# Kernel tuning notes

Hardware: AMD Instinct MI355X
Metric: run time of the kernel (lower is better)

## Reference

```python
import jax, jax.numpy as jnp
import numpy as np

V, E, H, T, B, F, D = 50000, 300, 256, 512, 64, 128, 256


def setup_inputs() -> dict:
    key = jax.random.key(0)
    ks = jax.random.split(key, 28)
    def g(i, shape, s=0.05):
        return jax.random.normal(ks[i], shape, jnp.float32) * s
    return {
        "tokens": jax.random.randint(ks[0], (B, T), 0, V, dtype=jnp.int32),
        "lengths": jax.random.randint(ks[1], (B,), 16, T + 1, dtype=jnp.int32),
        "emb": g(2, (V, E), 0.1),
        "Wih_f": g(3, (4 * H, E)), "Whh_f": g(4, (4 * H, H)),
        "bih_f": g(5, (4 * H,)), "bhh_f": g(6, (4 * H,)),
        "Wih_b": g(7, (4 * H, E)), "Whh_b": g(8, (4 * H, H)),
        "bih_b": g(9, (4 * H,)), "bhh_b": g(10, (4 * H,)),
        "attn_w": g(11, (2 * H, 1)), "attn_b": g(12, (1,)),
        "conv_w3": g(13, (F, 2 * H, 3)), "conv_b3": g(14, (F,)),
        "conv_w5": g(15, (F, 2 * H, 5)), "conv_b5": g(16, (F,)),
        "conv_w7": g(17, (F, 2 * H, 7)), "conv_b7": g(18, (F,)),
        "conv_w9": g(19, (F, 2 * H, 9)), "conv_b9": g(20, (F,)),
        "fc1_w": g(21, (D, 4 * F)), "fc1_b": g(22, (D,)),
        "fc2_w": g(23, (1, D)), "fc2_b": g(24, (1,)),
    }


def _lstm(x, Wih, Whh, bih, bhh):
    # x: [T, B, E]; torch LSTM gate order i, f, g, o. Returns hidden states [T, B, H].
    Hd = Whh.shape[1]
    xg = jnp.einsum('tbe,ge->tbg', x, Wih) + bih + bhh  # precompute input projections
    def step(carry, g_t):
        h, c = carry
        g = g_t + h @ Whh.T
        i, f, gg, o = jnp.split(g, 4, axis=-1)
        c = jax.nn.sigmoid(f) * c + jax.nn.sigmoid(i) * jnp.tanh(gg)
        h = jax.nn.sigmoid(o) * jnp.tanh(c)
        return (h, c), h
    h0 = jnp.zeros((x.shape[1], Hd), x.dtype)
    _, hs = jax.lax.scan(step, (h0, h0), xg)
    return hs


def _conv1d(x, w, b):
    # x: [B, C, T], w: [F, C, k] -> [B, F, T-k+1]
    y = jax.lax.conv_general_dilated(x, w, (1,), 'VALID',
                                     dimension_numbers=('NCH', 'OIH', 'NCH'))
    return y + b[None, :, None]


def reference(tokens, lengths, emb, Wih_f, Whh_f, bih_f, bhh_f,
              Wih_b, Whh_b, bih_b, bhh_b, attn_w, attn_b,
              conv_w3, conv_b3, conv_w5, conv_b5, conv_w7, conv_b7,
              conv_w9, conv_b9, fc1_w, fc1_b, fc2_w, fc2_b):
    Tn = tokens.shape[1]
    x = emb[tokens].transpose(1, 0, 2)                         # [T, B, E]
    t_idx = jnp.arange(Tn)
    mask = (t_idx[:, None] < lengths[None, :]).astype(x.dtype)  # [T, B]
    # forward direction
    fwd = _lstm(x, Wih_f, Whh_f, bih_f, bhh_f)
    # backward direction: per-sequence reverse of the valid prefix (packed-sequence semantics)
    rev = jnp.where(mask > 0, lengths[None, :] - 1 - t_idx[:, None], t_idx[:, None])  # [T, B]
    x_rev = jnp.take_along_axis(x, rev[:, :, None], axis=0)
    bwd = jnp.take_along_axis(_lstm(x_rev, Wih_b, Whh_b, bih_b, bhh_b), rev[:, :, None], axis=0)
    h = jnp.concatenate([fwd, bwd], axis=-1)                   # [T, B, 2H]
    # per-sequence softmax attention over valid timesteps (exp-normalize as in source)
    u = jnp.tanh(h) @ attn_w + attn_b                          # [T, B, 1]
    e = jnp.exp(u[..., 0]) * mask                              # [T, B]
    ctx = e / jnp.sum(e, axis=0, keepdims=True)
    r = h * ctx[..., None]                                     # zero at padded steps -> ZeroPad2d to max_len
    cnn_in = r.transpose(1, 2, 0)                              # [B, 2H, max_len]
    pooled = [jnp.max(_conv1d(cnn_in, w, b), axis=-1)
              for w, b in ((conv_w3, conv_b3), (conv_w5, conv_b5),
                           (conv_w7, conv_b7), (conv_w9, conv_b9))]
    cat = jnp.concatenate(pooled, axis=1)                      # [B, 4F]
    out = jax.nn.relu(cat @ fc1_w.T + fc1_b)
    out = jax.nn.sigmoid(out @ fc2_w.T + fc2_b)
    return out.reshape(-1, 1)
```

## Files before the change

kernel.cpp:

```cpp
#include <hip/hip_runtime.h>
#include <stdint.h>

typedef __attribute__((ext_vector_type(4))) float f32x4;
typedef __attribute__((ext_vector_type(8))) short s16x8;
typedef __attribute__((ext_vector_type(4))) unsigned short us4;

__device__ __forceinline__ float b2f(unsigned short h) {
    union { unsigned int u; float f; } v; v.u = ((unsigned int)h) << 16; return v.f;
}
__device__ __forceinline__ unsigned short f2b(float f) {
    union { float f; unsigned int u; } v; v.f = f;
    unsigned int u = v.u;
    unsigned int r = (u + 0x7FFFu + ((u >> 16) & 1u)) >> 16;
    return (unsigned short)r;
}
__device__ __forceinline__ f32x4 mfma_bf16(s16x8 a, s16x8 b, f32x4 c) {
    return __builtin_amdgcn_mfma_f32_16x16x32_bf16(a, b, c, 0, 0, 0);
}
__device__ __forceinline__ float fast_rcp(float x) {
    return __builtin_amdgcn_rcpf(x);
}
__device__ __forceinline__ float sigm(float x) {
    return fast_rcp(1.f + __expf(-x));
}
__device__ __forceinline__ float tanh_ap(float x) {
    float e = __expf(2.f * x);
    return 1.f - 2.f * fast_rcp(e + 1.f);
}
__device__ __forceinline__ unsigned int mapf(float f) {
    union { float f; unsigned int u; } v; v.f = f;
    return (v.u & 0x80000000u) ? ~v.u : (v.u | 0x80000000u);
}

#define TT 512
#define BB 64
#define EE 300
#define EPAD 320
#define HH 256
#define G4 1024
#define TP 520

__global__ void prep_w(const float* __restrict__ Wih_f, const float* __restrict__ Wih_b,
                       const float* __restrict__ Whh_f, const float* __restrict__ Whh_b,
                       const float* __restrict__ bih_f, const float* __restrict__ bhh_f,
                       const float* __restrict__ bih_b, const float* __restrict__ bhh_b,
                       unsigned short* __restrict__ Wb_f, unsigned short* __restrict__ Wb_b,
                       unsigned short* __restrict__ Whhb_f, unsigned short* __restrict__ Whhb_b,
                       float* __restrict__ bias_f, float* __restrict__ bias_b)
{
    int idx = blockIdx.x * 256 + threadIdx.x;
    if (idx < 327680) {
        int n = idx / EPAD, k = idx % EPAD;
        Wb_f[idx] = f2b(k < EE ? Wih_f[n * EE + k] : 0.f);
    } else if (idx < 655360) {
        int i = idx - 327680; int n = i / EPAD, k = i % EPAD;
        Wb_b[i] = f2b(k < EE ? Wih_b[n * EE + k] : 0.f);
    } else if (idx < 917504) {
        int i = idx - 655360; Whhb_f[i] = f2b(Whh_f[i]);
    } else if (idx < 1179648) {
        int i = idx - 917504; Whhb_b[i] = f2b(Whh_b[i]);
    } else if (idx < 1180672) {
        int i = idx - 1179648; bias_f[i] = bih_f[i] + bhh_f[i];
    } else if (idx < 1181696) {
        int i = idx - 1180672; bias_b[i] = bih_b[i] + bhh_b[i];
    }
}

__global__ void wcat_prep(const float* __restrict__ w3, const float* __restrict__ w5,
                          const float* __restrict__ w7, const float* __restrict__ w9,
                          unsigned short* __restrict__ Wcat)
{
    int idx = blockIdx.x * 256 + threadIdx.x;
    if (idx >= 512 * 4608) return;
    int f = idx / 4608, kk = idx - f * 4608;
    int j = kk >> 9, c = kk & 511;
    int g = f >> 7, fl = f & 127;
    int kw = 3 + 2 * g;
    const float* src = (g == 0) ? w3 : ((g == 1) ? w5 : ((g == 2) ? w7 : w9));
    float v = (j < kw) ? src[((size_t)fl * 512 + c) * kw + j] : 0.f;
    Wcat[idx] = f2b(v);
}

__global__ void build_A(const int* __restrict__ tokens, const int* __restrict__ lengths,
                        const float* __restrict__ emb,
                        unsigned short* __restrict__ A_f, unsigned short* __restrict__ A_b)
{
    int idx = blockIdx.x * 256 + threadIdx.x;
    const int per = 32768 * 40;
    if (idx >= 2 * per) return;
    int dirc = idx >= per;
    int rem = dirc ? idx - per : idx;
    int row = rem / 40, kc = (rem - row * 40) * 8;
    int t = row >> 6, b = row & 63;
    int ts = t;
    if (dirc) { int len = lengths[b]; ts = (t < len) ? (len - 1 - t) : t; }
    int tok = tokens[b * TT + ts];
    const float* ep = emb + (size_t)tok * EE;
    unsigned short* dst = (dirc ? A_b : A_f) + (size_t)row * EPAD + kc;
#pragma unroll
    for (int j2 = 0; j2 < 8; ++j2) {
        int e = kc + j2;
        dst[j2] = f2b(e < EE ? ep[e] : 0.f);
    }
}

__global__ void pool_init(unsigned int* __restrict__ p) {
    int idx = blockIdx.x * 256 + threadIdx.x;
    if (idx < 64 * 512) p[idx] = 0x007FFFFFu;
}

__global__ void zero_r(unsigned short* __restrict__ r) {
    int idx = blockIdx.x * 256 + threadIdx.x;
    if (idx >= 64 * 8 * 512) return;
    int b = idx >> 12;
    int rem = idx & 4095;
    r[((size_t)b * TP + 512) * 512 + rem] = 0;
}

__global__ __launch_bounds__(256) void gemm_xg_k(
    const unsigned short* __restrict__ A, const unsigned short* __restrict__ Bw,
    const float* __restrict__ bias, unsigned short* __restrict__ C)
{
    __shared__ unsigned short As[128][72];
    __shared__ unsigned short Bs[128][72];
    const int KA = EPAD;
    int tid = threadIdx.x;
    int row0 = blockIdx.x * 128, col0 = blockIdx.y * 128;
    int lane = tid & 63, wave = tid >> 6;
    int wr = (wave >> 1) * 64, wc = (wave & 1) * 64;
    int l15 = lane & 15, lg = lane >> 4;
    f32x4 acc[4][4] = {};
    for (int k0 = 0; k0 < KA; k0 += 64) {
        for (int ci = tid; ci < 1024; ci += 256) {
            int rr = ci >> 3, kc = (ci & 7) * 8;
            *(s16x8*)(&As[rr][kc]) = *(const s16x8*)(A + (size_t)(row0 + rr) * KA + k0 + kc);
            *(s16x8*)(&Bs[rr][kc]) = *(const s16x8*)(Bw + (size_t)(col0 + rr) * KA + k0 + kc);
        }
        __syncthreads();
#pragma unroll
        for (int kk = 0; kk < 64; kk += 32) {
            s16x8 af[4], bf[4];
#pragma unroll
            for (int m = 0; m < 4; ++m) af[m] = *(const s16x8*)(&As[wr + m * 16 + l15][kk + lg * 8]);
#pragma unroll
            for (int n = 0; n < 4; ++n) bf[n] = *(const s16x8*)(&Bs[wc + n * 16 + l15][kk + lg * 8]);
#pragma unroll
            for (int m = 0; m < 4; ++m)
#pragma unroll
                for (int n = 0; n < 4; ++n)
                    acc[m][n] = mfma_bf16(af[m], bf[n], acc[m][n]);
        }
        __syncthreads();
    }
    int t = (row0 + wr) >> 6;
#pragma unroll
    for (int m = 0; m < 4; ++m)
#pragma unroll
        for (int n = 0; n < 4; ++n) {
            int ccol = col0 + wc + n * 16 + l15;
            float bb = bias[ccol];
            us4 pk;
#pragma unroll
            for (int i = 0; i < 4; ++i) pk[i] = f2b(acc[m][n][i] + bb);
            size_t us4_idx = (((size_t)t * 4 + m) * 1024 + ccol) * 4 + lg;
            *(us4*)(C + us4_idx * 4) = pk;
        }
}

#define LSTM_STEP(S, XCUR, XNXT, HC, HW)                                          \
{                                                                                 \
    _Pragma("unroll")                                                             \
    for (int ct = 0; ct < 8; ++ct)                                                \
        wl2a[ct] = *(const s16x8*)(wbase + coff[ct] + 6 * 32);                    \
    f32x4 acc[8];                                                                 \
    _Pragma("unroll")                                                             \
    for (int ct = 0; ct < 8; ++ct) {                                              \
        f32x4 a;                                                                  \
        _Pragma("unroll")                                                         \
        for (int i = 0; i < 4; ++i) a[i] = b2f(XCUR[ct][i]);                      \
        acc[ct] = a;                                                              \
    }                                                                             \
    __syncthreads();              \
    s16x8 af[8];                                                                  \
    _Pragma("unroll")                                                             \
    for (int kt = 0; kt < 8; ++kt) af[kt] = *(const s16x8*)((HC) + kt * 32);      \
    _Pragma("unroll")                                                             \
    for (int kt = 0; kt < 4; ++kt)                                                \
        _Pragma("unroll")                                                         \
        for (int ct = 0; ct < 8; ++ct)                                            \
            acc[ct] = mfma_bf16(af[kt], wreg[ct * 4 + kt], acc[ct]);              \
    _Pragma("unroll")                                                             \
    for (int ct = 0; ct < 8; ++ct)                                                \
        wl2b[ct] = *(const s16x8*)(wbase + coff[ct] + 7 * 32);                    \
    _Pragma("unroll")                                                             \
    for (int ktl = 0; ktl < 2; ++ktl)                                             \
        _Pragma("unroll")                                                         \
        for (int ct = 0; ct < 8; ++ct)                                            \
            acc[ct] = mfma_bf16(af[4 + ktl], w_lds[wave][ktl][ct][lane], acc[ct]);\
    {                                                                             \
        int sp1 = (S) + 1; if (sp1 > 511) sp1 = 511;                              \
        const unsigned short* xs = xbase + (size_t)sp1 * 65536;                   \
        XNXT[0] = *(const us4*)(xs);                                              \
        XNXT[1] = *(const us4*)(xs + 256);                                        \
        XNXT[2] = *(const us4*)(xs + 4096);                                       \
        XNXT[3] = *(const us4*)(xs + 4352);                                       \
        XNXT[4] = *(const us4*)(xs + 8192);                                       \
        XNXT[5] = *(const us4*)(xs + 8448);                                       \
        XNXT[6] = *(const us4*)(xs + 12288);                                      \
        XNXT[7] = *(const us4*)(xs + 12544);                                      \
    }                                                                             \
    _Pragma("unroll")                                                             \
    for (int ct = 0; ct < 8; ++ct) acc[ct] = mfma_bf16(af[6], wl2a[ct], acc[ct]); \
    _Pragma("unroll")                                                             \
    for (int ct = 0; ct < 8; ++ct) acc[ct] = mfma_bf16(af[7], wl2b[ct], acc[ct]); \
    _Pragma("unroll")                                                             \
    for (int h2 = 0; h2 < 2; ++h2)                                                \
    _Pragma("unroll")                                                             \
    for (int i = 0; i < 4; ++i) {                                                 \
        int bi = lg * 4 + i;                                                      \
        int u = wave * 32 + h2 * 16 + l15;                                        \
        float gi = acc[0 + h2][i], gf = acc[2 + h2][i];                           \
        float gg = acc[4 + h2][i], go = acc[6 + h2][i];                           \
        float si = sigm(gi), sf = sigm(gf), so = sigm(go);                        \
        float tg = tanh_ap(gg);                                                   \
        int q = h2 * 4 + i;                                                       \
        float cc = sf * c[q] + si * tg; c[q] = cc;                                \
        float hh = so * tanh_ap(cc);                                              \
        (HW)[bi][u] = f2b(hh);                                                    \
        int len = len_s[bi];                                                      \
        if ((S) < len) {                                                          \
            int t_out = dir ? (len - 1 - (S)) : (S);                              \
            hs[((size_t)t_out * 64 + (grp * 16 + bi)) * 512 + dir * 256 + u] = f2b(hh); \
        }                                                                         \
    }                                                                             \
}

__global__ __launch_bounds__(512, 2) void lstm_rec(
    const unsigned short* __restrict__ xg_f, const unsigned short* __restrict__ xg_b,
    const unsigned short* __restrict__ Whh_fb, const unsigned short* __restrict__ Whh_bb,
    const int* __restrict__ lengths, unsigned short* __restrict__ hs)
{
    int wg = blockIdx.x;
    int dir = wg >> 2, grp = wg & 3;
    const unsigned short* XG = dir ? xg_b : xg_f;
    const unsigned short* WH = dir ? Whh_bb : Whh_fb;
    int tid = threadIdx.x, lane = tid & 63, wave = tid >> 6;
    int l15 = lane & 15, lg = lane >> 4;

    __shared__ unsigned short h_a[2][16][264];
    __shared__ s16x8 w_lds[8][2][8][64];
    __shared__ int len_s[16];
    __shared__ int ml_s;

    if (tid < 16) len_s[tid] = lengths[grp * 16 + tid];
    for (int i = tid; i < 2 * 16 * 264; i += 512) (&h_a[0][0][0])[i] = 0;
    __syncthreads();
    if (tid == 0) {
        int m = 0;
        for (int i = 0; i < 16; ++i) m = max(m, len_s[i]);
        ml_s = m;
    }

    const unsigned short* wbase = WH + (size_t)(wave * 32 + l15) * HH + lg * 8;
    const int coff[8] = {0, 16 * HH, 256 * HH, 272 * HH, 512 * HH, 528 * HH, 768 * HH, 784 * HH};

    s16x8 wreg[32];
#pragma unroll
    for (int ct = 0; ct < 8; ++ct) {
#pragma unroll
        for (int kt = 0; kt < 4; ++kt)
            wreg[ct * 4 + kt] = *(const s16x8*)(wbase + coff[ct] + kt * 32);
#pragma unroll
        for (int ktl = 0; ktl < 2; ++ktl)
            w_lds[wave][ktl][ct][lane] = *(const s16x8*)(wbase + coff[ct] + (4 + ktl) * 32);
    }
    __syncthreads();
    int maxlen = ml_s;

    float c[8];
#pragma unroll
    for (int q = 0; q < 8; ++q) c[q] = 0.f;

    const unsigned short* hc0 = &h_a[0][l15][lg * 8];
    const unsigned short* hc1 = &h_a[1][l15][lg * 8];
    const unsigned short* xbase = XG + (size_t)grp * 16384 + (wave * 32 + l15) * 16 + lg * 4;

    s16x8 wl2a[8], wl2b[8];
    us4 xga[8], xgb[8];
    {
        const unsigned short* xs = xbase;
        xga[0] = *(const us4*)(xs);         xga[1] = *(const us4*)(xs + 256);
        xga[2] = *(const us4*)(xs + 4096);  xga[3] = *(const us4*)(xs + 4352);
        xga[4] = *(const us4*)(xs + 8192);  xga[5] = *(const us4*)(xs + 8448);
        xga[6] = *(const us4*)(xs + 12288); xga[7] = *(const us4*)(xs + 12544);
    }

    int s = 0;
    for (; s + 1 < maxlen; s += 2) {
        LSTM_STEP(s, xga, xgb, hc0, h_a[1])
        LSTM_STEP(s + 1, xgb, xga, hc1, h_a[0])
    }
    if (s < maxlen) {
        LSTM_STEP(s, xga, xgb, hc0, h_a[1])
    }
}

__global__ __launch_bounds__(256) void attn_k(
    const unsigned short* __restrict__ hs, const int* __restrict__ lengths,
    const float* __restrict__ attn_w, unsigned short* __restrict__ r)
{
    int b = blockIdx.x, tid = threadIdx.x;
    __shared__ float aw[512];
    __shared__ float e_s[512];
    __shared__ float red[4];
    __shared__ float ssum;
    for (int i = tid; i < 512; i += 256) aw[i] = attn_w[i];
    int len = lengths[b];
    __syncthreads();
    for (int t = tid; t < 512; t += 256) {
        float e = 0.f;
        if (t < len) {
            const unsigned short* hp = hs + ((size_t)t * 64 + b) * 512;
            float u = 0.f;
            for (int c8 = 0; c8 < 64; ++c8) {
                s16x8 hv = *(const s16x8*)(hp + c8 * 8);
#pragma unroll
                for (int j = 0; j < 8; ++j)
                    u += tanh_ap(b2f((unsigned short)hv[j])) * aw[c8 * 8 + j];
            }
            e = __expf(u);
        }
        e_s[t] = e;
    }
    __syncthreads();
    float p = e_s[tid] + e_s[tid + 256];
#pragma unroll
    for (int o = 32; o > 0; o >>= 1) p += __shfl_down(p, o);
    if ((tid & 63) == 0) red[tid >> 6] = p;
    __syncthreads();
    if (tid == 0) ssum = red[0] + red[1] + red[2] + red[3];
    __syncthreads();
    float inv = fast_rcp(ssum);
    for (int idx = tid; idx < 512 * 512; idx += 256) {
        int t = idx >> 9, c = idx & 511;
        unsigned short outv = 0;
        if (t < len) {
            float scale = e_s[t] * inv;
            outv = f2b(b2f(hs[((size_t)t * 64 + b) * 512 + c]) * scale);
        }
        r[((size_t)b * TP + t) * 512 + c] = outv;
    }
}

__global__ __launch_bounds__(256) void gemm_conv(
    const unsigned short* __restrict__ R, const unsigned short* __restrict__ W,
    unsigned int* __restrict__ pooled)
{
    __shared__ unsigned short As[128][72];
    __shared__ unsigned short Bs[128][72];
    int tid = threadIdx.x;
    int bm = blockIdx.x;
    int b = bm >> 2;
    int t0 = (bm & 3) * 128;
    int col0 = blockIdx.y * 128;
    int kmax = (3 + 2 * (int)blockIdx.y) * 512;
    int lane = tid & 63, wave = tid >> 6;
    int wr = (wave >> 1) * 64, wc = (wave & 1) * 64;
    int l15 = lane & 15, lg = lane >> 4;
    f32x4 acc[4][4] = {};
    for (int k0 = 0; k0 < kmax; k0 += 64) {
        int j = k0 >> 9, c0 = k0 & 511;
        for (int ci = tid; ci < 1024; ci += 256) {
            int rr = ci >> 3, kc = (ci & 7) * 8;
            *(s16x8*)(&As[rr][kc]) =
                *(const s16x8*)(R + ((size_t)(b * TP) + t0 + rr + j) * 512 + c0 + kc);
            *(s16x8*)(&Bs[rr][kc]) = *(const s16x8*)(W + (size_t)(col0 + rr) * 4608 + k0 + kc);
        }
        __syncthreads();
#pragma unroll
        for (int kk = 0; kk < 64; kk += 32) {
            s16x8 af[4], bf[4];
#pragma unroll
            for (int m = 0; m < 4; ++m) af[m] = *(const s16x8*)(&As[wr + m * 16 + l15][kk + lg * 8]);
#pragma unroll
            for (int n = 0; n < 4; ++n) bf[n] = *(const s16x8*)(&Bs[wc + n * 16 + l15][kk + lg * 8]);
#pragma unroll
            for (int m = 0; m < 4; ++m)
#pragma unroll
                for (int n = 0; n < 4; ++n)
                    acc[m][n] = mfma_bf16(af[m], bf[n], acc[m][n]);
        }
        __syncthreads();
    }
#pragma unroll
    for (int m = 0; m < 4; ++m)
#pragma unroll
        for (int n = 0; n < 4; ++n) {
            int f = col0 + wc + n * 16 + l15;
            int g = f >> 7;
            int tmax = 509 - 2 * g;
            float v = -3.4e38f;
            int tb = t0 + wr + m * 16 + lg * 4;
#pragma unroll
            for (int i = 0; i < 4; ++i) {
                int t = tb + i;
                if (t <= tmax) v = fmaxf(v, acc[m][n][i]);
            }
            v = fmaxf(v, __shfl_xor(v, 16));
            v = fmaxf(v, __shfl_xor(v, 32));
            if (lane < 16) atomicMax(&pooled[b * 512 + f], mapf(v));
        }
}

__global__ __launch_bounds__(256) void fc_k(
    const unsigned int* __restrict__ pooled,
    const float* __restrict__ cb3, const float* __restrict__ cb5,
    const float* __restrict__ cb7, const float* __restrict__ cb9,
    const float* __restrict__ fc1_w, const float* __restrict__ fc1_b,
    const float* __restrict__ fc2_w, const float* __restrict__ fc2_b,
    float* __restrict__ out)
{
    int b = blockIdx.x, tid = threadIdx.x;
    __shared__ float x[512];
    __shared__ float y[256];
    for (int i = tid; i < 512; i += 256) {
        unsigned int u = pooled[b * 512 + i];
        unsigned int bits = (u & 0x80000000u) ? (u & 0x7FFFFFFFu) : ~u;
        union { unsigned int uu; float f; } v; v.uu = bits;
        int g = i >> 7;
        const float* cb = (g == 0) ? cb3 : ((g == 1) ? cb5 : ((g == 2) ? cb7 : cb9));
        x[i] = v.f + cb[i & 127];
    }
    __syncthreads();
    float a = fc1_b[tid];
    const float* wrow = fc1_w + (size_t)tid * 512;
    for (int k = 0; k < 512; k += 4)
        a += x[k] * wrow[k] + x[k + 1] * wrow[k + 1] + x[k + 2] * wrow[k + 2] + x[k + 3] * wrow[k + 3];
    y[tid] = fmaxf(a, 0.f);
    __syncthreads();
    if (tid < 64) {
        float p = 0.f;
        for (int k = tid; k < 256; k += 64) p += y[k] * fc2_w[k];
#pragma unroll
        for (int o = 32; o > 0; o >>= 1) p += __shfl_down(p, o);
        if (tid == 0) out[b] = 1.f / (1.f + __expf(-(p + fc2_b[0])));
    }
}

extern "C" void kernel_launch(void* const* d_in, const int* in_sizes, int n_in,
                              void* d_out, int out_size, void* d_ws, size_t ws_size,
                              hipStream_t stream)
{
    const int*   tokens  = (const int*)d_in[0];
    const int*   lengths = (const int*)d_in[1];
    const float* emb     = (const float*)d_in[2];
    const float* Wih_f   = (const float*)d_in[3];
    const float* Whh_f   = (const float*)d_in[4];
    const float* bih_f   = (const float*)d_in[5];
    const float* bhh_f   = (const float*)d_in[6];
    const float* Wih_b   = (const float*)d_in[7];
    const float* Whh_b   = (const float*)d_in[8];
    const float* bih_b   = (const float*)d_in[9];
    const float* bhh_b   = (const float*)d_in[10];
    const float* attn_w  = (const float*)d_in[11];
    const float* cw3 = (const float*)d_in[13]; const float* cb3 = (const float*)d_in[14];
    const float* cw5 = (const float*)d_in[15]; const float* cb5 = (const float*)d_in[16];
    const float* cw7 = (const float*)d_in[17]; const float* cb7 = (const float*)d_in[18];
    const float* cw9 = (const float*)d_in[19]; const float* cb9 = (const float*)d_in[20];
    const float* fc1_w = (const float*)d_in[21]; const float* fc1_b = (const float*)d_in[22];
    const float* fc2_w = (const float*)d_in[23]; const float* fc2_b = (const float*)d_in[24];
    float* out = (float*)d_out;

    char* ws = (char*)d_ws;
    unsigned short* A_f    = (unsigned short*)(ws + 0);
    unsigned short* A_b    = (unsigned short*)(ws + 20971520);
    unsigned short* r      = (unsigned short*)(ws + 0);
    unsigned short* Wb_f   = (unsigned short*)(ws + 41943040);
    unsigned short* Wb_b   = (unsigned short*)(ws + 42598400);
    unsigned short* Whhb_f = (unsigned short*)(ws + 43253760);
    unsigned short* Whhb_b = (unsigned short*)(ws + 43778048);
    float*          bias_f = (float*)(ws + 44302336);
    float*          bias_b = (float*)(ws + 44306432);
    unsigned short* Wcat   = (unsigned short*)(ws + 44310528);
    unsigned int*   pooled = (unsigned int*)(ws + 49029120);
    unsigned short* xg_f   = (unsigned short*)(ws + 49160192);
    unsigned short* xg_b   = (unsigned short*)(ws + 116269056);
    unsigned short* hs     = (unsigned short*)(ws + 183377920);

    prep_w<<<(1181696 + 255) / 256, 256, 0, stream>>>(Wih_f, Wih_b, Whh_f, Whh_b,
        bih_f, bhh_f, bih_b, bhh_b, Wb_f, Wb_b, Whhb_f, Whhb_b, bias_f, bias_b);
    wcat_prep<<<(2359296 + 255) / 256, 256, 0, stream>>>(cw3, cw5, cw7, cw9, Wcat);
    build_A<<<(2621440 + 255) / 256, 256, 0, stream>>>(tokens, lengths, emb, A_f, A_b);
    pool_init<<<128, 256, 0, stream>>>(pooled);

    gemm_xg_k<<<dim3(256, 8), 256, 0, stream>>>(A_f, Wb_f, bias_f, xg_f);
    gemm_xg_k<<<dim3(256, 8), 256, 0, stream>>>(A_b, Wb_b, bias_b, xg_b);

    lstm_rec<<<8, 512, 0, stream>>>(xg_f, xg_b, Whhb_f, Whhb_b, lengths, hs);

    zero_r<<<(262144 + 255) / 256, 256, 0, stream>>>(r);
    attn_k<<<64, 256, 0, stream>>>(hs, lengths, attn_w, r);

    gemm_conv<<<dim3(256, 4), 256, 0, stream>>>(r, Wcat, pooled);

    fc_k<<<64, 256, 0, stream>>>(pooled, cb3, cb5, cb7, cb9,
                                 fc1_w, fc1_b, fc2_w, fc2_b, out);
}
```

Baseline: 2.180 ms.

## Split LSTM recurrence across 16 waves with 16 hidden units each

Doubles the lstm_rec workgroup from 512 to 1024 threads so each wave owns 16 hidden units (4 gate tiles) instead of 32 (8 gate tiles). Each wave then issues half as many MFMAs and loads per timestep, which shortens the serial per-step critical path of the recurrence. The cost is more waves contending at the per-step barrier. Register budget per thread must also fit the higher launch bound, which could force spills.

```diff
diff --git a/kernel.cpp b/kernel.cpp
--- a/kernel.cpp
+++ b/kernel.cpp
@@ -170,11 +170,11 @@
 #define LSTM_STEP(S, XCUR, XNXT, HC, HW)                                          \
 {                                                                                 \
     _Pragma("unroll")                                                             \
-    for (int ct = 0; ct < 8; ++ct)                                                \
-        wl2a[ct] = *(const s16x8*)(wbase + coff[ct] + 6 * 32);                    \
-    f32x4 acc[8];                                                                 \
-    _Pragma("unroll")                                                             \
-    for (int ct = 0; ct < 8; ++ct) {                                              \
+    for (int ct = 0; ct < 4; ++ct)                                                \
+        wl2a[ct] = *(const s16x8*)(wbase + ct * 65536 + 6 * 32);                  \
+    f32x4 acc[4];                                                                 \
+    _Pragma("unroll")                                                             \
+    for (int ct = 0; ct < 4; ++ct) {                                              \
         f32x4 a;                                                                  \
         _Pragma("unroll")                                                         \
         for (int i = 0; i < 4; ++i) a[i] = b2f(XCUR[ct][i]);                      \
@@ -187,55 +187,46 @@
     _Pragma("unroll")                                                             \
     for (int kt = 0; kt < 4; ++kt)                                                \
         _Pragma("unroll")                                                         \
-        for (int ct = 0; ct < 8; ++ct)                                            \
+        for (int ct = 0; ct < 4; ++ct)                                            \
             acc[ct] = mfma_bf16(af[kt], wreg[ct * 4 + kt], acc[ct]);              \
     _Pragma("unroll")                                                             \
-    for (int ct = 0; ct < 8; ++ct)                                                \
-        wl2b[ct] = *(const s16x8*)(wbase + coff[ct] + 7 * 32);                    \
+    for (int ct = 0; ct < 4; ++ct)                                                \
+        wl2b[ct] = *(const s16x8*)(wbase + ct * 65536 + 7 * 32);                  \
     _Pragma("unroll")                                                             \
     for (int ktl = 0; ktl < 2; ++ktl)                                             \
         _Pragma("unroll")                                                         \
-        for (int ct = 0; ct < 8; ++ct)                                            \
+        for (int ct = 0; ct < 4; ++ct)                                            \
             acc[ct] = mfma_bf16(af[4 + ktl], w_lds[wave][ktl][ct][lane], acc[ct]);\
     {                                                                             \
         int sp1 = (S) + 1; if (sp1 > 511) sp1 = 511;                              \
         const unsigned short* xs = xbase + (size_t)sp1 * 65536;                   \
         XNXT[0] = *(const us4*)(xs);                                              \
-        XNXT[1] = *(const us4*)(xs + 256);                                        \
-        XNXT[2] = *(const us4*)(xs + 4096);                                       \
-        XNXT[3] = *(const us4*)(xs + 4352);                                       \
-        XNXT[4] = *(const us4*)(xs + 8192);                                       \
-        XNXT[5] = *(const us4*)(xs + 8448);                                       \
-        XNXT[6] = *(const us4*)(xs + 12288);                                      \
-        XNXT[7] = *(const us4*)(xs + 12544);                                      \
+        XNXT[1] = *(const us4*)(xs + 4096);                                       \
+        XNXT[2] = *(const us4*)(xs + 8192);                                       \
+        XNXT[3] = *(const us4*)(xs + 12288);                                      \
     }                                                                             \
     _Pragma("unroll")                                                             \
-    for (int ct = 0; ct < 8; ++ct) acc[ct] = mfma_bf16(af[6], wl2a[ct], acc[ct]); \
-    _Pragma("unroll")                                                             \
-    for (int ct = 0; ct < 8; ++ct) acc[ct] = mfma_bf16(af[7], wl2b[ct], acc[ct]); \
-    _Pragma("unroll")                                                             \
-    for (int h2 = 0; h2 < 2; ++h2)                                                \
+    for (int ct = 0; ct < 4; ++ct) acc[ct] = mfma_bf16(af[6], wl2a[ct], acc[ct]); \
+    _Pragma("unroll")                                                             \
+    for (int ct = 0; ct < 4; ++ct) acc[ct] = mfma_bf16(af[7], wl2b[ct], acc[ct]); \
     _Pragma("unroll")                                                             \
     for (int i = 0; i < 4; ++i) {                                                 \
         int bi = lg * 4 + i;                                                      \
-        int u = wave * 32 + h2 * 16 + l15;                                        \
-        float gi = acc[0 + h2][i], gf = acc[2 + h2][i];                           \
-        float gg = acc[4 + h2][i], go = acc[6 + h2][i];                           \
+        float gi = acc[0][i], gf = acc[1][i], gg = acc[2][i], go = acc[3][i];     \
         float si = sigm(gi), sf = sigm(gf), so = sigm(go);                        \
         float tg = tanh_ap(gg);                                                   \
-        int q = h2 * 4 + i;                                                       \
-        float cc = sf * c[q] + si * tg; c[q] = cc;                                \
+        float cc = sf * c[i] + si * tg; c[i] = cc;                                \
         float hh = so * tanh_ap(cc);                                              \
-        (HW)[bi][u] = f2b(hh);                                                    \
+        (HW)[bi][u_col] = f2b(hh);                                                \
         int len = len_s[bi];                                                      \
         if ((S) < len) {                                                          \
             int t_out = dir ? (len - 1 - (S)) : (S);                              \
-            hs[((size_t)t_out * 64 + (grp * 16 + bi)) * 512 + dir * 256 + u] = f2b(hh); \
+            hs[((size_t)t_out * 64 + (grp * 16 + bi)) * 512 + dir * 256 + u_col] = f2b(hh); \
         }                                                                         \
     }                                                                             \
 }
 
-__global__ __launch_bounds__(512, 2) void lstm_rec(
+__global__ __launch_bounds__(1024, 4) void lstm_rec(
     const unsigned short* __restrict__ xg_f, const unsigned short* __restrict__ xg_b,
     const unsigned short* __restrict__ Whh_fb, const unsigned short* __restrict__ Whh_bb,
     const int* __restrict__ lengths, unsigned short* __restrict__ hs)
@@ -246,14 +237,15 @@
     const unsigned short* WH = dir ? Whh_bb : Whh_fb;
     int tid = threadIdx.x, lane = tid & 63, wave = tid >> 6;
     int l15 = lane & 15, lg = lane >> 4;
+    int u_col = wave * 16 + l15;
 
     __shared__ unsigned short h_a[2][16][264];
-    __shared__ s16x8 w_lds[8][2][8][64];
+    __shared__ s16x8 w_lds[16][2][4][64];
     __shared__ int len_s[16];
     __shared__ int ml_s;
 
     if (tid < 16) len_s[tid] = lengths[grp * 16 + tid];
-    for (int i = tid; i < 2 * 16 * 264; i += 512) (&h_a[0][0][0])[i] = 0;
+    for (int i = tid; i < 2 * 16 * 264; i += 1024) (&h_a[0][0][0])[i] = 0;
     __syncthreads();
     if (tid == 0) {
         int m = 0;
@@ -261,38 +253,37 @@
         ml_s = m;
     }
 
-    const unsigned short* wbase = WH + (size_t)(wave * 32 + l15) * HH + lg * 8;
-    const int coff[8] = {0, 16 * HH, 256 * HH, 272 * HH, 512 * HH, 528 * HH, 768 * HH, 784 * HH};
-
-    s16x8 wreg[32];
-#pragma unroll
-    for (int ct = 0; ct < 8; ++ct) {
+    const unsigned short* wbase = WH + (size_t)u_col * HH + lg * 8;
+
+    s16x8 wreg[16];
+#pragma unroll
+    for (int ct = 0; ct < 4; ++ct) {
 #pragma unroll
         for (int kt = 0; kt < 4; ++kt)
-            wreg[ct * 4 + kt] = *(const s16x8*)(wbase + coff[ct] + kt * 32);
+            wreg[ct * 4 + kt] = *(const s16x8*)(wbase + ct * 65536 + kt * 32);
 #pragma unroll
         for (int ktl = 0; ktl < 2; ++ktl)
-            w_lds[wave][ktl][ct][lane] = *(const s16x8*)(wbase + coff[ct] + (4 + ktl) * 32);
+            w_lds[wave][ktl][ct][lane] = *(const s16x8*)(wbase + ct * 65536 + (4 + ktl) * 32);
     }
     __syncthreads();
     int maxlen = ml_s;
 
-    float c[8];
-#pragma unroll
-    for (int q = 0; q < 8; ++q) c[q] = 0.f;
+    float c[4];
+#pragma unroll
+    for (int q = 0; q < 4; ++q) c[q] = 0.f;
 
     const unsigned short* hc0 = &h_a[0][l15][lg * 8];
     const unsigned short* hc1 = &h_a[1][l15][lg * 8];
-    const unsigned short* xbase = XG + (size_t)grp * 16384 + (wave * 32 + l15) * 16 + lg * 4;
-
-    s16x8 wl2a[8], wl2b[8];
-    us4 xga[8], xgb[8];
+    const unsigned short* xbase = XG + (size_t)grp * 16384 + (size_t)u_col * 16 + lg * 4;
+
+    s16x8 wl2a[4], wl2b[4];
+    us4 xga[4], xgb[4];
     {
         const unsigned short* xs = xbase;
-        xga[0] = *(const us4*)(xs);         xga[1] = *(const us4*)(xs + 256);
-        xga[2] = *(const us4*)(xs + 4096);  xga[3] = *(const us4*)(xs + 4352);
-        xga[4] = *(const us4*)(xs + 8192);  xga[5] = *(const us4*)(xs + 8448);
-        xga[6] = *(const us4*)(xs + 12288); xga[7] = *(const us4*)(xs + 12544);
+        xga[0] = *(const us4*)(xs);
+        xga[1] = *(const us4*)(xs + 4096);
+        xga[2] = *(const us4*)(xs + 8192);
+        xga[3] = *(const us4*)(xs + 12288);
     }
 
     int s = 0;
@@ -496,7 +487,7 @@
     gemm_xg_k<<<dim3(256, 8), 256, 0, stream>>>(A_f, Wb_f, bias_f, xg_f);
     gemm_xg_k<<<dim3(256, 8), 256, 0, stream>>>(A_b, Wb_b, bias_b, xg_b);
 
-    lstm_rec<<<8, 512, 0, stream>>>(xg_f, xg_b, Whhb_f, Whhb_b, lengths, hs);
+    lstm_rec<<<8, 1024, 0, stream>>>(xg_f, xg_b, Whhb_f, Whhb_b, lengths, hs);
 
     zero_r<<<(262144 + 255) / 256, 256, 0, stream>>>(r);
     attn_k<<<64, 256, 0, stream>>>(hs, lengths, attn_w, r);
```

New measurement: 2.403 ms. 10.2% more time.
